# Optimization experiments

Hardware: AMD Instinct MI355X
Metric: run time of the kernel (lower is better)

## Reference

```python
import jax, jax.numpy as jnp
import numpy as np

N = 32
R = 128  # num_regions
F = 128  # num_features


def setup_inputs() -> dict:
    key = jax.random.key(0)
    k1, k2, k3, k4 = jax.random.split(key, 4)
    x1 = jax.random.normal(k1, (N, R * F), dtype=jnp.float32)
    x2 = jax.random.normal(k2, (N, R * F), dtype=jnp.float32)
    sigma = jax.random.normal(k3, (1,), dtype=jnp.float32) * 100.0
    mean = jax.random.normal(k4, (1,), dtype=jnp.float32)
    return {"x1": x1, "x2": x2, "sigma": sigma, "mean": mean}


def reference(x1, x2, sigma, mean):
    # (N, R, 1, F) - (N, 1, R, F) - mean -> (N, R, R, F)
    a = x1.reshape(N, R, 1, F)
    b = x2.reshape(N, 1, R, F)
    diff = a - b - mean  # mean is shape (1,), broadcasts over F
    distance_squared = jnp.sum(diff * diff, axis=-1)  # (N, R, R)
    kernel_value = jnp.exp(-distance_squared / (2.0 * sigma[0] ** 2))
    return jax.nn.softmax(kernel_value, axis=-1)
```

## Files before the change

### kernel.cpp

```cpp
#include <hip/hip_runtime.h>

#define NB 32
#define RR 128
#define FF 128
#define FT 32
#define SB 132

__global__ __launch_bounds__(256) void gauss_fused(const float* __restrict__ x1,
                                                   const float* __restrict__ x2,
                                                   const float* __restrict__ sigma,
                                                   const float* __restrict__ mean,
                                                   float* __restrict__ out) {
  __shared__ __align__(16) float sh_b[FT * SB];
  __shared__ __align__(16) float sh_a[8 * FF];

  const int bid = blockIdx.x;
  const int n = bid >> 4;
  const int i0 = (bid & 15) << 3;
  const int tid = threadIdx.x;
  const int tx = tid & 31;
  const int ty = tid >> 5;

  const float mval = mean[0];
  const float sg = sigma[0];
  const float cneg = -1.0f / (2.0f * sg * sg);

  {
    const float4 v = ((const float4*)(x1 + (size_t)(n * RR + i0) * FF))[tid];
    ((float4*)sh_a)[tid] = make_float4(v.x - mval, v.y - mval, v.z - mval, v.w - mval);
  }

  const float* __restrict__ x2base = x2 + (size_t)n * RR * FF;
  const int jj = tid >> 3;
  const int fo = (tid & 7) << 2;

  float acc0 = 0.f, acc1 = 0.f, acc2 = 0.f, acc3 = 0.f;
  const int j0 = tx << 2;
  const float* __restrict__ arow = sh_a + ty * FF;

  for (int t = 0; t < FF / FT; ++t) {
    const int ftw = t * FT;
    __syncthreads();
#pragma unroll
    for (int p = 0; p < 4; ++p) {
      const int j = jj + p * 32;
      const float4 v = *(const float4*)(x2base + (size_t)j * FF + ftw + fo);
      sh_b[(fo + 0) * SB + j] = v.x;
      sh_b[(fo + 1) * SB + j] = v.y;
      sh_b[(fo + 2) * SB + j] = v.z;
      sh_b[(fo + 3) * SB + j] = v.w;
    }
    __syncthreads();

#pragma unroll
    for (int f = 0; f < FT; ++f) {
      const float4 b = *(const float4*)(sh_b + f * SB + j0);
      const float a = arow[ftw + f];
      float d;
      d = a - b.x; acc0 = fmaf(d, d, acc0);
      d = a - b.y; acc1 = fmaf(d, d, acc1);
      d = a - b.z; acc2 = fmaf(d, d, acc2);
      d = a - b.w; acc3 = fmaf(d, d, acc3);
    }
  }

  const float k0 = __expf(acc0 * cneg);
  const float k1 = __expf(acc1 * cneg);
  const float k2 = __expf(acc2 * cneg);
  const float k3 = __expf(acc3 * cneg);

  float mx = fmaxf(fmaxf(k0, k1), fmaxf(k2, k3));
#pragma unroll
  for (int off = 16; off >= 1; off >>= 1) mx = fmaxf(mx, __shfl_xor(mx, off, 64));
  const float e0 = __expf(k0 - mx);
  const float e1 = __expf(k1 - mx);
  const float e2 = __expf(k2 - mx);
  const float e3 = __expf(k3 - mx);
  float ssum = e0 + e1 + e2 + e3;
#pragma unroll
  for (int off = 16; off >= 1; off >>= 1) ssum += __shfl_xor(ssum, off, 64);
  const float r = 1.0f / ssum;

  *(float4*)(out + (size_t)(n * RR + i0 + ty) * RR + j0) =
      make_float4(e0 * r, e1 * r, e2 * r, e3 * r);
}

extern "C" void kernel_launch(void* const* d_in, const int* in_sizes, int n_in,
                              void* d_out, int out_size, void* d_ws, size_t ws_size,
                              hipStream_t stream) {
  const float* x1 = (const float*)d_in[0];
  const float* x2 = (const float*)d_in[1];
  const float* sigma = (const float*)d_in[2];
  const float* mean = (const float*)d_in[3];
  float* out = (float*)d_out;
  (void)d_ws; (void)ws_size;

  gauss_fused<<<dim3(NB * 16), dim3(256), 0, stream>>>(x1, x2, sigma, mean, out);
}
```

Baseline: 69.07 us.

## Expand squared distance into norms plus dot product with larger row tiles

Rewrites ||a-b-m||^2 as ||a-m||^2 + ||b+m||^2 - 2a·b. Per-row norms are computed once in the prologue, so the inner loop becomes a pure FMA dot product. Each block now handles 16 rows instead of 8, with x2 staged in two 64-feature halves in row-major padded shared memory. A-rows are read directly from global memory, and softmax drops the max subtraction because the kernel values lie in (0,1]. The expansion can lose accuracy through cancellation when distances are small relative to the norms, and the grid halves to 256 blocks.

```diff
diff --git a/kernel.cpp b/kernel.cpp
--- a/kernel.cpp
+++ b/kernel.cpp
@@ -3,86 +3,115 @@
 #define NB 32
 #define RR 128
 #define FF 128
-#define FT 32
-#define SB 132
+#define FH 64
+#define SBJ 68
 
-__global__ __launch_bounds__(256) void gauss_fused(const float* __restrict__ x1,
-                                                   const float* __restrict__ x2,
-                                                   const float* __restrict__ sigma,
-                                                   const float* __restrict__ mean,
-                                                   float* __restrict__ out) {
-  __shared__ __align__(16) float sh_b[FT * SB];
-  __shared__ __align__(16) float sh_a[8 * FF];
+__global__ __launch_bounds__(256) void gauss_v3(const float* __restrict__ x1,
+                                                const float* __restrict__ x2,
+                                                const float* __restrict__ sigma,
+                                                const float* __restrict__ mean,
+                                                float* __restrict__ out) {
+  __shared__ __align__(16) float sh_b[RR * SBJ];
+  __shared__ float sh_red[256];
+  __shared__ float sh_ca[16];
+  __shared__ float sh_cb[RR];
 
+  const int tid = threadIdx.x;
   const int bid = blockIdx.x;
-  const int n = bid >> 4;
-  const int i0 = (bid & 15) << 3;
-  const int tid = threadIdx.x;
-  const int tx = tid & 31;
-  const int ty = tid >> 5;
+  const int n = bid >> 3;
+  const int i0 = (bid & 7) << 4;
 
   const float mval = mean[0];
   const float sg = sigma[0];
   const float cneg = -1.0f / (2.0f * sg * sg);
+  const float m2 = 2.0f * mval;
 
   {
-    const float4 v = ((const float4*)(x1 + (size_t)(n * RR + i0) * FF))[tid];
-    ((float4*)sh_a)[tid] = make_float4(v.x - mval, v.y - mval, v.z - mval, v.w - mval);
+    const int r = tid >> 4, p = tid & 15;
+    const float4* src = (const float4*)(x1 + ((size_t)(n * RR + i0 + r)) * FF + p * 8);
+    const float4 v0 = src[0], v1 = src[1];
+    sh_red[tid] = v0.x * (v0.x - m2) + v0.y * (v0.y - m2) + v0.z * (v0.z - m2) +
+                  v0.w * (v0.w - m2) + v1.x * (v1.x - m2) + v1.y * (v1.y - m2) +
+                  v1.z * (v1.z - m2) + v1.w * (v1.w - m2);
+  }
+  __syncthreads();
+  if (tid < 16) {
+    float s = 0.f;
+#pragma unroll
+    for (int p = 0; p < 16; ++p) s += sh_red[tid * 16 + p];
+    sh_ca[tid] = s + (float)FF * mval * mval;
   }
 
-  const float* __restrict__ x2base = x2 + (size_t)n * RR * FF;
-  const int jj = tid >> 3;
-  const int fo = (tid & 7) << 2;
+  const int lane = tid & 63;
+  const int wv = __builtin_amdgcn_readfirstlane(tid >> 6);
+  const float* __restrict__ arow0 = x1 + ((size_t)(n * RR + i0 + wv * 4)) * FF;
 
-  float acc0 = 0.f, acc1 = 0.f, acc2 = 0.f, acc3 = 0.f;
-  const int j0 = tx << 2;
-  const float* __restrict__ arow = sh_a + ty * FF;
+  const int js = tid >> 1;
+  const int fo = (tid & 1) << 5;
+  const float* __restrict__ x2n = x2 + (size_t)n * RR * FF;
 
-  for (int t = 0; t < FF / FT; ++t) {
-    const int ftw = t * FT;
+  float acc[4][2] = {{0.f, 0.f}, {0.f, 0.f}, {0.f, 0.f}, {0.f, 0.f}};
+  float cbp = 0.f;
+
+  for (int h = 0; h < 2; ++h) {
     __syncthreads();
+    {
+      const float4* src = (const float4*)(x2n + (size_t)js * FF + h * FH + fo);
+      float4* dst = (float4*)(sh_b + js * SBJ + fo);
 #pragma unroll
-    for (int p = 0; p < 4; ++p) {
-      const int j = jj + p * 32;
-      const float4 v = *(const float4*)(x2base + (size_t)j * FF + ftw + fo);
-      sh_b[(fo + 0) * SB + j] = v.x;
-      sh_b[(fo + 1) * SB + j] = v.y;
-      sh_b[(fo + 2) * SB + j] = v.z;
-      sh_b[(fo + 3) * SB + j] = v.w;
+      for (int c = 0; c < 8; ++c) {
+        const float4 v = src[c];
+        dst[c] = v;
+        cbp += v.x * (v.x + m2) + v.y * (v.y + m2) + v.z * (v.z + m2) + v.w * (v.w + m2);
+      }
     }
     __syncthreads();
 
+    const float4* __restrict__ b0 = (const float4*)(sh_b + lane * SBJ);
+    const float4* __restrict__ b1 = (const float4*)(sh_b + (lane + 64) * SBJ);
 #pragma unroll
-    for (int f = 0; f < FT; ++f) {
-      const float4 b = *(const float4*)(sh_b + f * SB + j0);
-      const float a = arow[ftw + f];
-      float d;
-      d = a - b.x; acc0 = fmaf(d, d, acc0);
-      d = a - b.y; acc1 = fmaf(d, d, acc1);
-      d = a - b.z; acc2 = fmaf(d, d, acc2);
-      d = a - b.w; acc3 = fmaf(d, d, acc3);
+    for (int fq = 0; fq < FH / 4; ++fq) {
+      const float4 v0 = b0[fq];
+      const float4 v1 = b1[fq];
+#pragma unroll
+      for (int r = 0; r < 4; ++r) {
+        const float4 a = *(const float4*)(arow0 + r * FF + h * FH + fq * 4);
+        acc[r][0] = fmaf(a.x, v0.x, acc[r][0]);
+        acc[r][0] = fmaf(a.y, v0.y, acc[r][0]);
+        acc[r][0] = fmaf(a.z, v0.z, acc[r][0]);
+        acc[r][0] = fmaf(a.w, v0.w, acc[r][0]);
+        acc[r][1] = fmaf(a.x, v1.x, acc[r][1]);
+        acc[r][1] = fmaf(a.y, v1.y, acc[r][1]);
+        acc[r][1] = fmaf(a.z, v1.z, acc[r][1]);
+        acc[r][1] = fmaf(a.w, v1.w, acc[r][1]);
+      }
     }
   }
 
-  const float k0 = __expf(acc0 * cneg);
-  const float k1 = __expf(acc1 * cneg);
-  const float k2 = __expf(acc2 * cneg);
-  const float k3 = __expf(acc3 * cneg);
+  {
+    const float other = __shfl_xor(cbp, 1, 64);
+    if ((tid & 1) == 0) sh_cb[js] = cbp + other;
+  }
+  __syncthreads();
 
-  float mx = fmaxf(fmaxf(k0, k1), fmaxf(k2, k3));
+  const int j1 = lane + 64;
+  const float cb0 = sh_cb[lane];
+  const float cb1 = sh_cb[j1];
+  float* __restrict__ orow = out + ((size_t)(n * RR + i0 + wv * 4)) * RR;
 #pragma unroll
-  for (int off = 16; off >= 1; off >>= 1) mx = fmaxf(mx, __shfl_xor(mx, off, 64));
-  const float e0 = __expf(k0 - mx);
-  const float e1 = __expf(k1 - mx);
-  const float e2 = __expf(k2 - mx);
-  const float e3 = __expf(k3 - mx);
-  float ssum = e0 + e1 + e2 + e3;
+  for (int r = 0; r < 4; ++r) {
+    const float ca = sh_ca[wv * 4 + r];
+    const float k0 = __expf(cneg * (ca + cb0 - 2.f * acc[r][0]));
+    const float k1 = __expf(cneg * (ca + cb1 - 2.f * acc[r][1]));
+    const float e0 = __expf(k0);
+    const float e1 = __expf(k1);
+    float s = e0 + e1;
 #pragma unroll
-  for (int off = 16; off >= 1; off >>= 1) ssum += __shfl_xor(ssum, off, 64);
-  const float r = 1.0f / ssum;
-
-  *(float4*)(out + (size_t)(n * RR + i0 + ty) * RR + j0) =
-      make_float4(e0 * r, e1 * r, e2 * r, e3 * r);
+    for (int off = 32; off >= 1; off >>= 1) s += __shfl_xor(s, off, 64);
+    const float inv = 1.0f / s;
+    orow[r * RR + lane] = e0 * inv;
+    orow[r * RR + j1] = e1 * inv;
+  }
 }
 
 extern "C" void kernel_launch(void* const* d_in, const int* in_sizes, int n_in,
@@ -95,5 +124,5 @@
   float* out = (float*)d_out;
   (void)d_ws; (void)ws_size;
 
-  gauss_fused<<<dim3(NB * 16), dim3(256), 0, stream>>>(x1, x2, sigma, mean, out);
+  gauss_v3<<<dim3(NB * 8), dim3(256), 0, stream>>>(x1, x2, sigma, mean, out);
 }
```

Result: slower. 70.58 us (+2.2%).
